# Kernel optimization log

Hardware: AMD Instinct MI355X
Metric: run time of the kernel (lower is better)

## Reference

```python
import jax, jax.numpy as jnp
import numpy as np

N_NODES = 50000
N_EDGES = 800000
N_GRAPHS = 64
EPS = 1e-12


def setup_inputs() -> dict:
    key = jax.random.key(0)
    ks = jax.random.split(key, 8)
    x = jax.random.normal(ks[0], (N_NODES, 128), dtype=jnp.float32)
    edge_index = jax.random.randint(ks[1], (2, N_EDGES), 0, N_NODES, dtype=jnp.int64)
    batch = jnp.sort(jax.random.randint(ks[2], (N_NODES,), 0, N_GRAPHS, dtype=jnp.int64))
    W1 = jax.random.normal(ks[3], (128, 64), dtype=jnp.float32) * 0.1
    W2 = jax.random.normal(ks[4], (64, 64), dtype=jnp.float32) * 0.1
    W3 = jax.random.normal(ks[5], (64, 64), dtype=jnp.float32) * 0.1
    Wl = jax.random.normal(ks[6], (128, 32), dtype=jnp.float32) * 0.1
    return {
        'x': x, 'edge_index': edge_index, 'batch': batch,
        'W1': W1, 'b1': jnp.zeros((64,), jnp.float32),
        'W2': W2, 'b2': jnp.zeros((64,), jnp.float32),
        'W3': W3, 'b3': jnpp if False else jnp.zeros((64,), jnp.float32),
        'Wl': Wl, 'bl': jnp.zeros((32,), jnp.float32),
    }


def _gcn_conv(h, W, b, src, dst, dinv, enorm, n):
    # PyG GCNConv: D^-1/2 (A+I) D^-1/2 (h W) + b, self-loops included analytically
    hw = h @ W
    agg = jax.ops.segment_sum(hw[src] * enorm[:, None], dst, num_segments=n)
    agg = agg + (dinv * dinv)[:, None] * hw  # self-loop term
    return agg + b


def _norm_relu(h):
    # F.normalize(p=2, dim=1) then relu
    nrm = jnp.sqrt(jnp.sum(h * h, axis=1, keepdims=True))
    return jax.nn.relu(h / jnp.maximum(nrm, EPS))


def reference(x, edge_index, batch, W1, b1, W2, b2, W3, b3, Wl, bl):
    n = x.shape[0]
    src, dst = edge_index[0], edge_index[1]
    # degree with self-loops (counts incoming edges at target, +1 for self-loop)
    deg = jax.ops.segment_sum(jnp.ones((src.shape[0],), x.dtype), dst, num_segments=n) + 1.0
    dinv = 1.0 / jnp.sqrt(deg)
    enorm = dinv[src] * dinv[dst]

    h = _norm_relu(_gcn_conv(x, W1, b1, src, dst, dinv, enorm, n))
    h = _norm_relu(_gcn_conv(h, W2, b2, src, dst, dinv, enorm, n))
    h = _norm_relu(_gcn_conv(h, W3, b3, src, dst, dinv, enorm, n))

    counts = jax.ops.segment_sum(jnp.ones((n,), x.dtype), batch, num_segments=N_GRAPHS)
    x_mean = jax.ops.segment_sum(h, batch, num_segments=N_GRAPHS) / jnp.maximum(counts, 1.0)[:, None]
    x_max = jax.ops.segment_max(h, batch, num_segments=N_GRAPHS)
    x_max = jnp.where(counts[:, None] > 0, x_max, 0.0)  # guard empty graphs

    pooled = jnp.concatenate([x_mean, x_max], axis=-1)  # [B, 2*hidden]
    return pooled @ Wl + bl
```

## Files before the change

kernel.cpp:

```cpp
#include <hip/hip_runtime.h>
#include <hip/hip_bf16.h>

#define N_NODES 50000
#define N_EDGES 800000
#define N_GRAPHS 64
#define HID 64
#define SCAN_NB 196
#define FILL_RANGES 8
#define RANGE_SIZE ((N_NODES + FILL_RANGES - 1) / FILL_RANGES)

static inline size_t align256(size_t x) { return (x + 255) & ~(size_t)255; }

typedef __attribute__((ext_vector_type(8))) short short8v;
typedef __attribute__((ext_vector_type(4))) float f32x4;

__device__ __forceinline__ unsigned short f2bf(float f) {
    unsigned int u = __float_as_uint(f);
    unsigned int r = (u + 0x7fffu + ((u >> 16) & 1u)) >> 16;
    return (unsigned short)r;
}
__device__ __forceinline__ float bf2f(unsigned short h) {
    return __uint_as_float(((unsigned int)h) << 16);
}

__global__ void zero2(int* __restrict__ a, int na, int* __restrict__ b, int nb) {
    int i = blockIdx.x * blockDim.x + threadIdx.x;
    if (i < na) a[i] = 0;
    else if (i < na + nb) b[i - na] = 0;
}

__global__ void deg_kernel(const int* __restrict__ ei, int* __restrict__ cnt) {
    int e = blockIdx.x * blockDim.x + threadIdx.x;
    if (e < N_EDGES) atomicAdd(&cnt[ei[N_EDGES + e]], 1);
}

__global__ __launch_bounds__(256) void scan_a(const int* __restrict__ cnt,
                                              int* __restrict__ incl,
                                              int* __restrict__ bsum) {
    __shared__ int sd[256];
    int t = threadIdx.x;
    int i = blockIdx.x * 256 + t;
    int v = (i < N_NODES) ? cnt[i] : 0;
    sd[t] = v;
    __syncthreads();
    for (int off = 1; off < 256; off <<= 1) {
        int u = (t >= off) ? sd[t - off] : 0;
        __syncthreads();
        sd[t] += u;
        __syncthreads();
    }
    if (i < N_NODES) incl[i] = sd[t];
    if (t == 255) bsum[blockIdx.x] = sd[255];
}

__global__ __launch_bounds__(384) void scan_b_gstart(const int* __restrict__ bsum,
                                                     int* __restrict__ boff,
                                                     const int* __restrict__ batch,
                                                     int* __restrict__ gstart) {
    __shared__ int sd[256];
    int t = threadIdx.x;
    int v = 0;
    if (t < 256) {
        v = (t < SCAN_NB) ? bsum[t] : 0;
        sd[t] = v;
    }
    __syncthreads();
    for (int off = 1; off < 256; off <<= 1) {
        int u = (t < 256 && t >= off) ? sd[t - off] : 0;
        __syncthreads();
        if (t < 256) sd[t] += u;
        __syncthreads();
    }
    if (t < SCAN_NB) boff[t] = sd[t] - v;
    if (t >= 256 && t - 256 <= N_GRAPHS) {
        int g = t - 256;
        int lo = 0, hi = N_NODES;
        while (lo < hi) {
            int mid = (lo + hi) >> 1;
            if (batch[mid] < g) lo = mid + 1; else hi = mid;
        }
        gstart[g] = lo;
    }
}

__global__ void scan_c(const int* __restrict__ cnt, const int* __restrict__ incl,
                       const int* __restrict__ boff, int* __restrict__ row_ptr,
                       int* __restrict__ fill_ptr, float* __restrict__ dinv) {
    int i = blockIdx.x * blockDim.x + threadIdx.x;
    if (i < N_NODES) {
        int c = cnt[i];
        int run = boff[i >> 8] + incl[i];
        row_ptr[i + 1] = run;
        fill_ptr[i] = run - c;
        dinv[i] = rsqrtf((float)c + 1.0f);
        if (i == 0) row_ptr[0] = 0;
    }
}

__global__ __launch_bounds__(256) void fill_kernel(const int* __restrict__ ei,
                                                   int* __restrict__ fill_ptr,
                                                   int* __restrict__ csr_src) {
    int r = blockIdx.x & (FILL_RANGES - 1);
    int e = (blockIdx.x >> 3) * 256 + threadIdx.x;
    if (e >= N_EDGES) return;
    int dst = ei[N_EDGES + e];
    int lo = r * RANGE_SIZE;
    if (dst >= lo && dst < lo + RANGE_SIZE) {
        int src = ei[e];
        int pos = atomicAdd(&fill_ptr[dst], 1);
        csr_src[pos] = src;
    }
}

template <int K>
__global__ __launch_bounds__(256) void mfma_matmul(const float* __restrict__ h,
                                                   const float* __restrict__ W,
                                                   const float* __restrict__ dinv,
                                                   unsigned short* __restrict__ hw2) {
    constexpr int NSTEP = K / 32;
    __shared__ unsigned short sWH[NSTEP * 4 * 64 * 8];
    __shared__ unsigned short sWL[NSTEP * 4 * 64 * 8];
    int tid = threadIdx.x;
    int r0 = blockIdx.x * 64;

#pragma unroll 1
    for (int ent = tid; ent < NSTEP * 4 * 64; ent += 256) {
        int lane_e = ent & 63;
        int c = (ent >> 6) & 3;
        int step = ent >> 8;
        int kb = step * 32 + (lane_e >> 4) * 8;
        int n = c * 16 + (lane_e & 15);
#pragma unroll
        for (int j = 0; j < 8; ++j) {
            float f = W[(kb + j) * 64 + n];
            unsigned short hi = f2bf(f);
            sWH[ent * 8 + j] = hi;
            sWL[ent * 8 + j] = f2bf(f - bf2f(hi));
        }
    }
    __syncthreads();

    int lane = tid & 63;
    int wid = tid >> 6;
    int arow = min(r0 + wid * 16 + (lane & 15), N_NODES - 1);
    const float* ap = h + (size_t)arow * K;
    int klane = (lane >> 4) * 8;

    f32x4 acc[4];
#pragma unroll
    for (int c = 0; c < 4; ++c) acc[c] = (f32x4){0.f, 0.f, 0.f, 0.f};

#pragma unroll 1
    for (int step = 0; step < NSTEP; ++step) {
        int kb = step * 32 + klane;
        float4 f0 = *(const float4*)&ap[kb];
        float4 f1 = *(const float4*)&ap[kb + 4];
        float fv[8] = {f0.x, f0.y, f0.z, f0.w, f1.x, f1.y, f1.z, f1.w};
        short8v ahi, alo;
#pragma unroll
        for (int j = 0; j < 8; ++j) {
            unsigned short hi = f2bf(fv[j]);
            ahi[j] = (short)hi;
            alo[j] = (short)f2bf(fv[j] - bf2f(hi));
        }
#pragma unroll
        for (int c = 0; c < 4; ++c) {
            short8v bh = *(const short8v*)&sWH[((step * 4 + c) * 64 + lane) * 8];
            short8v bl = *(const short8v*)&sWL[((step * 4 + c) * 64 + lane) * 8];
            acc[c] = __builtin_amdgcn_mfma_f32_16x16x32_bf16(ahi, bh, acc[c], 0, 0, 0);
            acc[c] = __builtin_amdgcn_mfma_f32_16x16x32_bf16(alo, bh, acc[c], 0, 0, 0);
            acc[c] = __builtin_amdgcn_mfma_f32_16x16x32_bf16(ahi, bl, acc[c], 0, 0, 0);
        }
    }

    int rb = r0 + wid * 16 + (lane >> 4) * 4;
#pragma unroll
    for (int j = 0; j < 4; ++j) {
        int row = rb + j;
        if (row < N_NODES) {
            float dv = dinv[row];
#pragma unroll
            for (int c = 0; c < 4; ++c) {
                hw2[(size_t)row * 64 + c * 16 + (lane & 15)] = f2bf(dv * acc[c][j]);
            }
        }
    }
}

__global__ __launch_bounds__(256) void agg_kernel(const unsigned short* __restrict__ hw2,
                                                  const int* __restrict__ row_ptr,
                                                  const int* __restrict__ csr_src,
                                                  const float* __restrict__ dinv,
                                                  const float* __restrict__ b,
                                                  float* __restrict__ hout) {
    int node = blockIdx.x * 4 + (threadIdx.x >> 6);
    int lane = threadIdx.x & 63;
    if (node >= N_NODES) return;
    int grp = lane >> 3;
    int gl  = lane & 7;
    int s = row_ptr[node], e = row_ptr[node + 1];

    float acc[8] = {0.f, 0.f, 0.f, 0.f, 0.f, 0.f, 0.f, 0.f};
    for (int base = s; base < e; base += 64) {
        int nE = min(64, e - base);
        int msrc = (lane < nE) ? csr_src[base + lane] : 0;
#pragma unroll 2
        for (int i = 0; i < nE; i += 8) {
            int myi = i + grp;
            int src = __shfl(msrc, myi, 64);
            if (myi < nE) {
                short8v v = *(const short8v*)&hw2[(size_t)src * 64 + gl * 8];
#pragma unroll
                for (int j = 0; j < 8; ++j) acc[j] += bf2f((unsigned short)v[j]);
            }
        }
    }
#pragma unroll
    for (int off = 8; off <= 32; off <<= 1) {
#pragma unroll
        for (int j = 0; j < 8; ++j) acc[j] += __shfl_xor(acc[j], off, 64);
    }
    short8v sv = *(const short8v*)&hw2[(size_t)node * 64 + gl * 8];
#pragma unroll
    for (int j = 0; j < 8; ++j) acc[j] += bf2f((unsigned short)sv[j]);

    float di = dinv[node];
    float4 b0 = *(const float4*)&b[gl * 8];
    float4 b1 = *(const float4*)&b[gl * 8 + 4];
    float val[8];
    val[0] = di * acc[0] + b0.x;
    val[1] = di * acc[1] + b0.y;
    val[2] = di * acc[2] + b0.z;
    val[3] = di * acc[3] + b0.w;
    val[4] = di * acc[4] + b1.x;
    val[5] = di * acc[5] + b1.y;
    val[6] = di * acc[6] + b1.z;
    val[7] = di * acc[7] + b1.w;

    float sq = 0.f;
#pragma unroll
    for (int j = 0; j < 8; ++j) sq += val[j] * val[j];
#pragma unroll
    for (int off = 1; off <= 4; off <<= 1) sq += __shfl_xor(sq, off, 64);
    float inv = 1.0f / fmaxf(sqrtf(sq), 1e-12f);

    if (grp == 0) {
        float4 r0, r1;
        r0.x = fmaxf(val[0] * inv, 0.f);
        r0.y = fmaxf(val[1] * inv, 0.f);
        r0.z = fmaxf(val[2] * inv, 0.f);
        r0.w = fmaxf(val[3] * inv, 0.f);
        r1.x = fmaxf(val[4] * inv, 0.f);
        r1.y = fmaxf(val[5] * inv, 0.f);
        r1.z = fmaxf(val[6] * inv, 0.f);
        r1.w = fmaxf(val[7] * inv, 0.f);
        *(float4*)&hout[(size_t)node * 64 + gl * 8] = r0;
        *(float4*)&hout[(size_t)node * 64 + gl * 8 + 4] = r1;
    }
}

__global__ __launch_bounds__(256) void pool_partial_kernel(const float* __restrict__ h,
                                                           const int* __restrict__ batch,
                                                           float* __restrict__ gsum,
                                                           float* __restrict__ gmax) {
    int wid = threadIdx.x >> 6, lane = threadIdx.x & 63;
    int i0 = blockIdx.x * 64 + wid * 16;
    if (i0 >= N_NODES) return;
    int i1 = min(i0 + 16, N_NODES);
    int gcur = batch[i0];
    float sum = 0.f, mx = 0.f;
    for (int i = i0; i < i1; ++i) {
        int g = batch[i];
        if (g != gcur) {
            atomicAdd(&gsum[gcur * 64 + lane], sum);
            atomicMax((int*)&gmax[gcur * 64 + lane], __float_as_int(mx));
            sum = 0.f; mx = 0.f; gcur = g;
        }
        float v = h[(size_t)i * 64 + lane];
        sum += v;
        mx = fmaxf(mx, v);
    }
    atomicAdd(&gsum[gcur * 64 + lane], sum);
    atomicMax((int*)&gmax[gcur * 64 + lane], __float_as_int(mx));
}

__global__ __launch_bounds__(128) void linear_kernel(const float* __restrict__ gsum,
                                                     const float* __restrict__ gmax,
                                                     const int* __restrict__ gstart,
                                                     const float* __restrict__ Wl,
                                                     const float* __restrict__ bl,
                                                     float* __restrict__ out) {
    int g = blockIdx.x;
    __shared__ float pooled[128];
    int t = threadIdx.x;
    if (t < 64) {
        int cnt = gstart[g + 1] - gstart[g];
        pooled[t] = gsum[g * 64 + t] / fmaxf((float)cnt, 1.0f);
    } else {
        pooled[t] = gmax[g * 64 + (t - 64)];
    }
    __syncthreads();
    if (t < 32) {
        float acc = bl[t];
#pragma unroll 8
        for (int k = 0; k < 128; ++k) acc += pooled[k] * Wl[k * 32 + t];
        out[g * 32 + t] = acc;
    }
}

extern "C" void kernel_launch(void* const* d_in, const int* in_sizes, int n_in,
                              void* d_out, int out_size, void* d_ws, size_t ws_size,
                              hipStream_t stream) {
    const float* x        = (const float*)d_in[0];
    const int*   ei       = (const int*)d_in[1];
    const int*   batch    = (const int*)d_in[2];
    const float* W1       = (const float*)d_in[3];
    const float* b1       = (const float*)d_in[4];
    const float* W2       = (const float*)d_in[5];
    const float* b2       = (const float*)d_in[6];
    const float* W3       = (const float*)d_in[7];
    const float* b3       = (const float*)d_in[8];
    const float* Wl       = (const float*)d_in[9];
    const float* bl       = (const float*)d_in[10];
    float* out = (float*)d_out;

    char* ws = (char*)d_ws;
    int*   cnt      = (int*)ws;                 ws += align256((size_t)N_NODES * 4);
    int*   incl     = (int*)ws;                 ws += align256((size_t)N_NODES * 4);
    int*   bsum     = (int*)ws;                 ws += align256((size_t)SCAN_NB * 4);
    int*   boff     = (int*)ws;                 ws += align256((size_t)SCAN_NB * 4);
    int*   row_ptr  = (int*)ws;                 ws += align256((size_t)(N_NODES + 1) * 4);
    int*   fill_ptr = (int*)ws;                 ws += align256((size_t)N_NODES * 4);
    float* dinv     = (float*)ws;               ws += align256((size_t)N_NODES * 4);
    int*   gstart   = (int*)ws;                 ws += align256((size_t)(N_GRAPHS + 1) * 4);
    float* gsum     = (float*)ws;               ws += align256((size_t)N_GRAPHS * 64 * 4);
    float* gmax     = (float*)ws;               ws += align256((size_t)N_GRAPHS * 64 * 4);
    int*   csr_src  = (int*)ws;                 ws += align256((size_t)N_EDGES * 4);
    unsigned short* hwb = (unsigned short*)ws;  ws += align256((size_t)N_NODES * 64 * 2);
    float* h1       = (float*)ws;               ws += align256((size_t)N_NODES * 64 * 4);
    float* h2       = (float*)ws;               ws += align256((size_t)N_NODES * 64 * 4);

    hipLaunchKernelGGL(zero2, dim3((N_NODES + 2 * N_GRAPHS * 64 + 255) / 256), dim3(256), 0,
                       stream, cnt, N_NODES, (int*)gsum, 2 * N_GRAPHS * 64);
    hipLaunchKernelGGL(deg_kernel, dim3((N_EDGES + 255) / 256), dim3(256), 0, stream, ei, cnt);
    hipLaunchKernelGGL(scan_a, dim3(SCAN_NB), dim3(256), 0, stream, cnt, incl, bsum);
    hipLaunchKernelGGL(scan_b_gstart, dim3(1), dim3(384), 0, stream, bsum, boff, batch, gstart);
    hipLaunchKernelGGL(scan_c, dim3(SCAN_NB), dim3(256), 0, stream,
                       cnt, incl, boff, row_ptr, fill_ptr, dinv);
    hipLaunchKernelGGL(fill_kernel,
                       dim3(FILL_RANGES * ((N_EDGES + 255) / 256)), dim3(256), 0, stream,
                       ei, fill_ptr, csr_src);

    const int mm_grid = (N_NODES + 63) / 64;
    const int agg_grid = (N_NODES + 3) / 4;

    hipLaunchKernelGGL((mfma_matmul<128>), dim3(mm_grid), dim3(256), 0, stream, x, W1, dinv, hwb);
    hipLaunchKernelGGL(agg_kernel, dim3(agg_grid), dim3(256), 0, stream,
                       hwb, row_ptr, csr_src, dinv, b1, h1);
    hipLaunchKernelGGL((mfma_matmul<64>), dim3(mm_grid), dim3(256), 0, stream, h1, W2, dinv, hwb);
    hipLaunchKernelGGL(agg_kernel, dim3(agg_grid), dim3(256), 0, stream,
                       hwb, row_ptr, csr_src, dinv, b2, h2);
    hipLaunchKernelGGL((mfma_matmul<64>), dim3(mm_grid), dim3(256), 0, stream, h2, W3, dinv, hwb);
    hipLaunchKernelGGL(agg_kernel, dim3(agg_grid), dim3(256), 0, stream,
                       hwb, row_ptr, csr_src, dinv, b3, h1);

    hipLaunchKernelGGL(pool_partial_kernel, dim3((N_NODES + 63) / 64), dim3(256), 0, stream,
                       h1, batch, gsum, gmax);
    hipLaunchKernelGGL(linear_kernel, dim3(N_GRAPHS), dim3(128), 0, stream,
                       gsum, gmax, gstart, Wl, bl, out);
}
```

Measured before the change: 212.4 us.

## Fuse pooling into final aggregation and widen per-lane feature slice to 16

The aggregation kernel now has each lane handle 16 features (4 lanes per row, 16 edges in flight per wave) rather than 8, which changes the gather width and the reduction pattern. The last aggregation layer is templated to skip writing h to global memory. It instead reduces the block's four nodes through shared memory and issues graph-level sum and max atomics directly, removing the separate pool kernel and its read of h. In exchange it adds a __syncthreads, more atomics (one set per block of 4 nodes), and more accumulator registers per lane.

New measurement: 251.1 us. 18.2% more time.

```diff
diff --git a/kernel.cpp b/kernel.cpp
--- a/kernel.cpp
+++ b/kernel.cpp
@@ -187,101 +187,120 @@
     }
 }
 
+template <bool POOL>
 __global__ __launch_bounds__(256) void agg_kernel(const unsigned short* __restrict__ hw2,
                                                   const int* __restrict__ row_ptr,
                                                   const int* __restrict__ csr_src,
                                                   const float* __restrict__ dinv,
                                                   const float* __restrict__ b,
-                                                  float* __restrict__ hout) {
-    int node = blockIdx.x * 4 + (threadIdx.x >> 6);
-    int lane = threadIdx.x & 63;
-    if (node >= N_NODES) return;
-    int grp = lane >> 3;
-    int gl  = lane & 7;
+                                                  float* __restrict__ hout,
+                                                  const int* __restrict__ batch,
+                                                  float* __restrict__ gsum,
+                                                  float* __restrict__ gmax) {
+    __shared__ float sh[4][64];
+    int tid = threadIdx.x;
+    int node = blockIdx.x * 4 + (tid >> 6);
+    int lane = tid & 63;
+    int grp = lane >> 2;
+    int gl  = lane & 3;
     int s = row_ptr[node], e = row_ptr[node + 1];
 
-    float acc[8] = {0.f, 0.f, 0.f, 0.f, 0.f, 0.f, 0.f, 0.f};
+    float acc[16];
+#pragma unroll
+    for (int j = 0; j < 16; ++j) acc[j] = 0.f;
+
     for (int base = s; base < e; base += 64) {
         int nE = min(64, e - base);
         int msrc = (lane < nE) ? csr_src[base + lane] : 0;
 #pragma unroll 2
-        for (int i = 0; i < nE; i += 8) {
+        for (int i = 0; i < nE; i += 16) {
             int myi = i + grp;
             int src = __shfl(msrc, myi, 64);
             if (myi < nE) {
-                short8v v = *(const short8v*)&hw2[(size_t)src * 64 + gl * 8];
-#pragma unroll
-                for (int j = 0; j < 8; ++j) acc[j] += bf2f((unsigned short)v[j]);
-            }
-        }
-    }
-#pragma unroll
-    for (int off = 8; off <= 32; off <<= 1) {
-#pragma unroll
-        for (int j = 0; j < 8; ++j) acc[j] += __shfl_xor(acc[j], off, 64);
-    }
-    short8v sv = *(const short8v*)&hw2[(size_t)node * 64 + gl * 8];
-#pragma unroll
-    for (int j = 0; j < 8; ++j) acc[j] += bf2f((unsigned short)sv[j]);
+                short8v v0 = *(const short8v*)&hw2[(size_t)src * 64 + gl * 16];
+                short8v v1 = *(const short8v*)&hw2[(size_t)src * 64 + gl * 16 + 8];
+#pragma unroll
+                for (int j = 0; j < 8; ++j) acc[j] += bf2f((unsigned short)v0[j]);
+#pragma unroll
+                for (int j = 0; j < 8; ++j) acc[8 + j] += bf2f((unsigned short)v1[j]);
+            }
+        }
+    }
+#pragma unroll
+    for (int off = 4; off <= 32; off <<= 1) {
+#pragma unroll
+        for (int j = 0; j < 16; ++j) acc[j] += __shfl_xor(acc[j], off, 64);
+    }
+    short8v s0 = *(const short8v*)&hw2[(size_t)node * 64 + gl * 16];
+    short8v s1 = *(const short8v*)&hw2[(size_t)node * 64 + gl * 16 + 8];
+#pragma unroll
+    for (int j = 0; j < 8; ++j) acc[j] += bf2f((unsigned short)s0[j]);
+#pragma unroll
+    for (int j = 0; j < 8; ++j) acc[8 + j] += bf2f((unsigned short)s1[j]);
 
     float di = dinv[node];
-    float4 b0 = *(const float4*)&b[gl * 8];
-    float4 b1 = *(const float4*)&b[gl * 8 + 4];
-    float val[8];
-    val[0] = di * acc[0] + b0.x;
-    val[1] = di * acc[1] + b0.y;
-    val[2] = di * acc[2] + b0.z;
-    val[3] = di * acc[3] + b0.w;
-    val[4] = di * acc[4] + b1.x;
-    val[5] = di * acc[5] + b1.y;
-    val[6] = di * acc[6] + b1.z;
-    val[7] = di * acc[7] + b1.w;
+    float val[16];
+#pragma unroll
+    for (int q = 0; q < 4; ++q) {
+        float4 bb = *(const float4*)&b[gl * 16 + q * 4];
+        val[q * 4 + 0] = di * acc[q * 4 + 0] + bb.x;
+        val[q * 4 + 1] = di * acc[q * 4 + 1] + bb.y;
+        val[q * 4 + 2] = di * acc[q * 4 + 2] + bb.z;
+        val[q * 4 + 3] = di * acc[q * 4 + 3] + bb.w;
+    }
 
     float sq = 0.f;
 #pragma unroll
-    for (int j = 0; j < 8; ++j) sq += val[j] * val[j];
-#pragma unroll
-    for (int off = 1; off <= 4; off <<= 1) sq += __shfl_xor(sq, off, 64);
+    for (int j = 0; j < 16; ++j) sq += val[j] * val[j];
+#pragma unroll
+    for (int off = 1; off <= 2; off <<= 1) sq += __shfl_xor(sq, off, 64);
     float inv = 1.0f / fmaxf(sqrtf(sq), 1e-12f);
 
-    if (grp == 0) {
-        float4 r0, r1;
-        r0.x = fmaxf(val[0] * inv, 0.f);
-        r0.y = fmaxf(val[1] * inv, 0.f);
-        r0.z = fmaxf(val[2] * inv, 0.f);
-        r0.w = fmaxf(val[3] * inv, 0.f);
-        r1.x = fmaxf(val[4] * inv, 0.f);
-        r1.y = fmaxf(val[5] * inv, 0.f);
-        r1.z = fmaxf(val[6] * inv, 0.f);
-        r1.w = fmaxf(val[7] * inv, 0.f);
-        *(float4*)&hout[(size_t)node * 64 + gl * 8] = r0;
-        *(float4*)&hout[(size_t)node * 64 + gl * 8 + 4] = r1;
-    }
-}
-
-__global__ __launch_bounds__(256) void pool_partial_kernel(const float* __restrict__ h,
-                                                           const int* __restrict__ batch,
-                                                           float* __restrict__ gsum,
-                                                           float* __restrict__ gmax) {
-    int wid = threadIdx.x >> 6, lane = threadIdx.x & 63;
-    int i0 = blockIdx.x * 64 + wid * 16;
-    if (i0 >= N_NODES) return;
-    int i1 = min(i0 + 16, N_NODES);
-    int gcur = batch[i0];
-    float sum = 0.f, mx = 0.f;
-    for (int i = i0; i < i1; ++i) {
-        int g = batch[i];
-        if (g != gcur) {
-            atomicAdd(&gsum[gcur * 64 + lane], sum);
-            atomicMax((int*)&gmax[gcur * 64 + lane], __float_as_int(mx));
-            sum = 0.f; mx = 0.f; gcur = g;
-        }
-        float v = h[(size_t)i * 64 + lane];
-        sum += v;
-        mx = fmaxf(mx, v);
-    }
-    atomicAdd(&gsum[gcur * 64 + lane], sum);
-    atomicMax((int*)&gmax[gcur * 64 + lane], __float_as_int(mx));
+    if (POOL) {
+        if (grp == 0) {
+#pragma unroll
+            for (int q = 0; q < 4; ++q) {
+                float4 r;
+                r.x = fmaxf(val[q * 4 + 0] * inv, 0.f);
+                r.y = fmaxf(val[q * 4 + 1] * inv, 0.f);
+                r.z = fmaxf(val[q * 4 + 2] * inv, 0.f);
+                r.w = fmaxf(val[q * 4 + 3] * inv, 0.f);
+                *(float4*)&sh[tid >> 6][gl * 16 + q * 4] = r;
+            }
+        }
+        __syncthreads();
+        if (tid < 64) {
+            int nb = blockIdx.x * 4;
+            int gcur = batch[nb];
+            float runsum = 0.f, runmax = 0.f;
+#pragma unroll
+            for (int w = 0; w < 4; ++w) {
+                int g = batch[nb + w];
+                if (g != gcur) {
+                    atomicAdd(&gsum[gcur * 64 + tid], runsum);
+                    atomicMax((int*)&gmax[gcur * 64 + tid], __float_as_int(runmax));
+                    runsum = 0.f; runmax = 0.f; gcur = g;
+                }
+                float v = sh[w][tid];
+                runsum += v;
+                runmax = fmaxf(runmax, v);
+            }
+            atomicAdd(&gsum[gcur * 64 + tid], runsum);
+            atomicMax((int*)&gmax[gcur * 64 + tid], __float_as_int(runmax));
+        }
+    } else {
+        if (grp == 0) {
+#pragma unroll
+            for (int q = 0; q < 4; ++q) {
+                float4 r;
+                r.x = fmaxf(val[q * 4 + 0] * inv, 0.f);
+                r.y = fmaxf(val[q * 4 + 1] * inv, 0.f);
+                r.z = fmaxf(val[q * 4 + 2] * inv, 0.f);
+                r.w = fmaxf(val[q * 4 + 3] * inv, 0.f);
+                *(float4*)&hout[(size_t)node * 64 + gl * 16 + q * 4] = r;
+            }
+        }
+    }
 }
 
 __global__ __launch_bounds__(128) void linear_kernel(const float* __restrict__ gsum,
@@ -352,20 +371,18 @@
                        ei, fill_ptr, csr_src);
 
     const int mm_grid = (N_NODES + 63) / 64;
-    const int agg_grid = (N_NODES + 3) / 4;
+    const int agg_grid = N_NODES / 4;
 
     hipLaunchKernelGGL((mfma_matmul<128>), dim3(mm_grid), dim3(256), 0, stream, x, W1, dinv, hwb);
-    hipLaunchKernelGGL(agg_kernel, dim3(agg_grid), dim3(256), 0, stream,
-                       hwb, row_ptr, csr_src, dinv, b1, h1);
+    hipLaunchKernelGGL((agg_kernel<false>), dim3(agg_grid), dim3(256), 0, stream,
+                       hwb, row_ptr, csr_src, dinv, b1, h1, batch, gsum, gmax);
     hipLaunchKernelGGL((mfma_matmul<64>), dim3(mm_grid), dim3(256), 0, stream, h1, W2, dinv, hwb);
-    hipLaunchKernelGGL(agg_kernel, dim3(agg_grid), dim3(256), 0, stream,
-                       hwb, row_ptr, csr_src, dinv, b2, h2);
+    hipLaunchKernelGGL((agg_kernel<false>), dim3(agg_grid), dim3(256), 0, stream,
+                       hwb, row_ptr, csr_src, dinv, b2, h2, batch, gsum, gmax);
     hipLaunchKernelGGL((mfma_matmul<64>), dim3(mm_grid), dim3(256), 0, stream, h2, W3, dinv, hwb);
-    hipLaunchKernelGGL(agg_kernel, dim3(agg_grid), dim3(256), 0, stream,
-                       hwb, row_ptr, csr_src, dinv, b3, h1);
-
-    hipLaunchKernelGGL(pool_partial_kernel, dim3((N_NODES + 63) / 64), dim3(256), 0, stream,
-                       h1, batch, gsum, gmax);
+    hipLaunchKernelGGL((agg_kernel<true>), dim3(agg_grid), dim3(256), 0, stream,
+                       hwb, row_ptr, csr_src, dinv, b3, (float*)nullptr, batch, gsum, gmax);
+
     hipLaunchKernelGGL(linear_kernel, dim3(N_GRAPHS), dim3(128), 0, stream,
                        gsum, gmax, gstart, Wl, bl, out);
 }
```
